# Optimization experiments

Hardware: AMD Instinct MI355X
Metric: run time of the kernel (lower is better)

## Reference

```python
import jax, jax.numpy as jnp
import numpy as np

V, D, NB, K, T = 32000, 256, 4, 8, 16


def setup_inputs() -> dict:
    key = jax.random.key(0)
    k0, k1, k2, k3, k4, k5 = jax.random.split(key, 6)
    tokens = jax.random.randint(k0, (T,), 0, V, dtype=jnp.int32)
    embed = jax.random.normal(k1, (V, D), jnp.float32) * 0.02
    W = jax.random.normal(k2, (K, D, D), jnp.float32) / np.float32(np.sqrt(D))
    bubbles = jax.random.normal(k3, (K, NB, D), jnp.float32) * 1.5  # init_spread_foam scale=1.5
    # scalars = [noise_gate_logit, self_temperature_logit, memory_decay_base, novelty_sensitivity]
    scalars = jax.random.normal(k4, (4,), jnp.float32)
    noise = jax.random.normal(k5, (T, K, NB, D), jnp.float32)  # per-step per-foam perturbations
    return {"tokens": tokens, "embed": embed, "W": W, "bubbles": bubbles,
            "scalars": scalars, "noise": noise}


def reference(tokens, embed, W, bubbles, scalars, noise):
    noise_gate = jax.nn.sigmoid(scalars[0])
    temp = jnp.maximum(jnp.abs(scalars[1]), 0.01)   # self_temperature
    decay_base = scalars[2]                          # memory_decay_base
    sensitivity = jnp.abs(scalars[3])                # novelty_sensitivity
    nb = bubbles.shape[1]

    def step(memory, inp):                           # memory: (K, NB, D)
        tok, pert = inp
        x = embed[tok]                               # (D,)
        mm = memory.mean(axis=1)                     # (K, D) memory mean per foam
        mem_norm = jnp.linalg.norm(mm, axis=-1) + 1e-10
        x_norm = jnp.linalg.norm(x) + 1e-10
        dot = mm @ x                                 # (K,)
        novelty = jnp.where(mem_norm > 1e-8, 1.0 - dot / (x_norm * mem_norm), 1.0)
        decay = jax.nn.sigmoid(decay_base - sensitivity * novelty)   # (K,)
        xwm = x[None, :] + decay[:, None] * mm                        # (K, D)
        state_scale = jnp.linalg.norm(xwm, axis=-1) + 1e-10           # (K,)
        # LevyFoam equilibrium (stand-in): small per-foam matmul + bubble offsets
        eq = jnp.tanh(jnp.einsum('kd,kde->ke', xwm, W))[:, None, :] + bubbles  # (K, NB, D)
        eq = eq + noise_gate * pert * state_scale[:, None, None] * 0.01
        new_mem = decay[:, None, None] * memory + (1.0 - decay)[:, None, None] * eq
        m = eq / (jnp.linalg.norm(eq, axis=-1, keepdims=True) + 1e-10)
        rho = jnp.einsum('kbd,kbe->kde', m, m) / nb                   # (K, D, D)
        purity = jnp.sum(rho * jnp.swapaxes(rho, 1, 2), axis=(1, 2))  # tr(rho @ rho)
        w = jax.nn.softmax(purity / temp)                             # (K,)
        rho_self = jnp.einsum('k,kde->de', w, rho)                    # (D, D)
        eig = jnp.clip(jnp.linalg.eigvalsh(rho_self), 1e-12, None)
        eig = eig / eig.sum()
        # born rule over full vocab: diag(E rho E^T)
        logits = jnp.sum((embed @ rho_self) * embed, axis=-1)         # (V,)
        logp = jax.nn.log_softmax(logits)
        probs = jnp.exp(logp)
        S_rho = -jnp.sum(eig * jnp.clip(jnp.log(eig), -100.0, None))
        H_tok = -jnp.sum(probs * jnp.clip(logp, -100.0, None))
        return new_mem, (probs, rho_self, S_rho, H_tok, purity, w)

    mem0 = jnp.zeros((W.shape[0], nb, embed.shape[1]), embed.dtype)
    _, outs = jax.lax.scan(step, mem0, (tokens, noise))
    token_probs, rhos, S_rho, H_tokens, purities, weights = outs
    return token_probs, rhos, S_rho, H_tokens, purities, weights
```

## Files before the change

### kernel.cpp

```cpp
#include <hip/hip_runtime.h>
#include <hip/hip_fp16.h>

#define VV 32000
#define DD 256
#define TT 16

#define OUT_PROBS 0
#define OUT_RHO   512000
#define OUT_SRHO  1560576
#define OUT_H     1560592
#define OUT_PUR   1560608
#define OUT_W     1560672

#define WS_MS    0
#define WS_MSBF  65536
#define WS_G     98304
#define WS_MAXP  102400
#define WS_SUMP  106496
#define WS_C     110592
#define WS_EBF   131072

#define LAMZ 5.3e-4f

typedef __attribute__((ext_vector_type(8))) short s8v;
typedef __attribute__((ext_vector_type(8))) _Float16 h8v;
typedef __attribute__((ext_vector_type(4))) float f4v;

__device__ __forceinline__ unsigned short f2bf(float f) {
  unsigned u = __float_as_uint(f);
  u += 0x7fffu + ((u >> 16) & 1u);
  return (unsigned short)(u >> 16);
}

__device__ __forceinline__ float fast_sigmoid(float z) {
  return __builtin_amdgcn_rcpf(1.f + __expf(-z));
}
__device__ __forceinline__ float fast_tanh(float y) {
  return 1.f - 2.f * __builtin_amdgcn_rcpf(__expf(2.f * y) + 1.f);
}

__global__ __launch_bounds__(512, 1) void k_chains(
    const int* __restrict__ tokens, const float* __restrict__ embed,
    const float* __restrict__ W, const float* __restrict__ bubbles,
    const float* __restrict__ scalars, const float* __restrict__ noise,
    float* __restrict__ out, float* __restrict__ ws,
    unsigned short* __restrict__ ebf) {
  const int k = blockIdx.x;
  const int tid = threadIdx.x;

  if (k >= 4) {
    const float4* src = (const float4*)embed;
    size_t start = (size_t)(k - 4) * 4000;
    if (ebf) {
      #pragma unroll 4
      for (int i = tid; i < 4000; i += 512) {
        float4 v = src[start + i];
        ushort4 o;
        o.x = f2bf(v.x); o.y = f2bf(v.y); o.z = f2bf(v.z); o.w = f2bf(v.w);
        *(ushort4*)(ebf + (size_t)(start + i) * 4) = o;
      }
    } else {
      float a = 0.f;
      #pragma unroll 4
      for (int i = tid; i < 4000; i += 512) {
        float4 v = src[start + i];
        a += v.x + v.y + v.z + v.w;
      }
      asm volatile("" :: "v"(a));
    }
    return;
  }

  __shared__ __align__(16) float erow[16 * 256];
  __shared__ __align__(16) float s_ms[64 * 256];
  __shared__ __align__(16) char  s_nz[32768];
  __shared__ __align__(16) float s_mmv[256];
  __shared__ __align__(16) float s_eq[256];
  __shared__ float s_rp[12];
  __shared__ float s_pp[40];
  __shared__ float s_pur[16];

  if (tid >= 256) {
    const int u = tid - 256;
    #pragma unroll 4
    for (int t = 0; t < TT; ++t) {
      const float* np = noise + (size_t)((t * 4 + k) * 4) * 256 + u;
      float n0 = np[0], n1 = np[256], n2 = np[512], n3 = np[768];
      uint64_t pk = (uint64_t)f2bf(n0) | ((uint64_t)f2bf(n1) << 16) |
                    ((uint64_t)f2bf(n2) << 32) | ((uint64_t)f2bf(n3) << 48);
      *(uint64_t*)(s_nz + ((t * 256 + u) << 3)) = pk;
    }
    #pragma unroll
    for (int it = 0; it < 4; ++it) {
      int f = it * 256 + u;
      int row = f >> 6, c4 = (f & 63) << 2;
      int tok = tokens[row];
      *(float4*)&erow[row * 256 + c4] = *(const float4*)(embed + (size_t)tok * DD + c4);
    }
    __syncthreads();
    return;
  }

  const int l = tid & 63, w = tid >> 6, lg = l >> 4;
  h8v Wreg[4][8];
  {
    const float* wp = W + (size_t)k * 65536 + (size_t)lg * 8 * 256 + w * 64 + (l & 15);
    #pragma unroll
    for (int nt = 0; nt < 4; ++nt) {
      #pragma unroll
      for (int kk = 0; kk < 8; ++kk) {
        h8v b;
        #pragma unroll
        for (int j = 0; j < 8; ++j)
          b[j] = (_Float16)wp[(kk * 32 + j) * 256 + nt * 16];
        Wreg[nt][kk] = b;
      }
    }
  }
  float bub0 = bubbles[(k * 4 + 0) * DD + tid];
  float bub1 = bubbles[(k * 4 + 1) * DD + tid];
  float bub2 = bubbles[(k * 4 + 2) * DD + tid];
  float bub3 = bubbles[(k * 4 + 3) * DD + tid];
  const float noise_gate = fast_sigmoid(scalars[0]);
  const float decay_base = scalars[2];
  const float sens = fabsf(scalars[3]);
  const float rowmask = ((l & 15) == 0) ? 1.f : 0.f;
  float mem0 = 0.f, mem1 = 0.f, mem2 = 0.f, mem3 = 0.f;
  __syncthreads();

  #pragma unroll 1
  for (int t = 0; t < TT; ++t) {
    float x = erow[t * 256 + tid];
    float mmv = 0.25f * (mem0 + mem1 + mem2 + mem3);
    s_mmv[tid] = mmv;
    float r0 = mmv * x, r1 = mmv * mmv, r2 = x * x;
    #pragma unroll
    for (int mm = 32; mm; mm >>= 1) {
      r0 += __shfl_xor(r0, mm);
      r1 += __shfl_xor(r1, mm);
      r2 += __shfl_xor(r2, mm);
    }
    if (l == 0) { s_rp[w * 3] = r0; s_rp[w * 3 + 1] = r1; s_rp[w * 3 + 2] = r2; }
    __syncthreads();
    float dot = s_rp[0] + s_rp[3] + s_rp[6] + s_rp[9];
    float mn  = s_rp[1] + s_rp[4] + s_rp[7] + s_rp[10];
    float xn  = s_rp[2] + s_rp[5] + s_rp[8] + s_rp[11];
    float mem_norm = sqrtf(mn) + 1e-10f;
    float x_norm = sqrtf(xn) + 1e-10f;
    float novelty = (mem_norm > 1e-8f) ? (1.f - dot / (x_norm * mem_norm)) : 1.f;
    float decay = fast_sigmoid(decay_base - sens * novelty);
    float ss2 = xn + 2.f * decay * dot + decay * decay * mn;
    float state_scale = sqrtf(ss2) + 1e-10f;
    float cns = noise_gate * state_scale * 0.01f;

    uint64_t pk = *(const uint64_t*)(s_nz + ((t * 256 + tid) << 3));
    float nz0 = __uint_as_float((uint32_t)(pk & 0xFFFFu) << 16);
    float nz1 = __uint_as_float((uint32_t)((pk >> 16) & 0xFFFFu) << 16);
    float nz2 = __uint_as_float((uint32_t)((pk >> 32) & 0xFFFFu) << 16);
    float nz3 = __uint_as_float((uint32_t)(pk >> 48) << 16);

    h8v afr[8];
    #pragma unroll
    for (int kk = 0; kk < 8; ++kk) {
      const float* mp_ = s_mmv + kk * 32 + lg * 8;
      const float* xp_ = erow + t * 256 + kk * 32 + lg * 8;
      float4 mv0 = *(const float4*)mp_, mv1 = *(const float4*)(mp_ + 4);
      float4 xv0 = *(const float4*)xp_, xv1 = *(const float4*)(xp_ + 4);
      h8v a;
      a[0] = (_Float16)(fmaf(decay, mv0.x, xv0.x) * rowmask);
      a[1] = (_Float16)(fmaf(decay, mv0.y, xv0.y) * rowmask);
      a[2] = (_Float16)(fmaf(decay, mv0.z, xv0.z) * rowmask);
      a[3] = (_Float16)(fmaf(decay, mv0.w, xv0.w) * rowmask);
      a[4] = (_Float16)(fmaf(decay, mv1.x, xv1.x) * rowmask);
      a[5] = (_Float16)(fmaf(decay, mv1.y, xv1.y) * rowmask);
      a[6] = (_Float16)(fmaf(decay, mv1.z, xv1.z) * rowmask);
      a[7] = (_Float16)(fmaf(decay, mv1.w, xv1.w) * rowmask);
      afr[kk] = a;
    }
    f4v acc[4];
    #pragma unroll
    for (int nt = 0; nt < 4; ++nt) acc[nt] = (f4v){0.f, 0.f, 0.f, 0.f};
    #pragma unroll
    for (int kk = 0; kk < 8; ++kk) {
      #pragma unroll
      for (int nt = 0; nt < 4; ++nt)
        acc[nt] = __builtin_amdgcn_mfma_f32_16x16x32_f16(afr[kk], Wreg[nt][kk], acc[nt], 0, 0, 0);
    }
    if (l < 16) {
      s_eq[w * 64 + 0 * 16 + l] = acc[0][0];
      s_eq[w * 64 + 1 * 16 + l] = acc[1][0];
      s_eq[w * 64 + 2 * 16 + l] = acc[2][0];
      s_eq[w * 64 + 3 * 16 + l] = acc[3][0];
    }
    asm volatile("s_waitcnt lgkmcnt(0)" ::: "memory");
    __builtin_amdgcn_sched_barrier(0);
    float th = fast_tanh(s_eq[tid]);
    float eq0 = th + bub0 + cns * nz0;
    float eq1 = th + bub1 + cns * nz1;
    float eq2 = th + bub2 + cns * nz2;
    float eq3 = th + bub3 + cns * nz3;
    float p[10];
    p[0] = eq0 * eq0; p[1] = eq0 * eq1; p[2] = eq0 * eq2; p[3] = eq0 * eq3;
    p[4] = eq1 * eq1; p[5] = eq1 * eq2; p[6] = eq1 * eq3;
    p[7] = eq2 * eq2; p[8] = eq2 * eq3; p[9] = eq3 * eq3;
    #pragma unroll
    for (int mm = 32; mm; mm >>= 1) {
      #pragma unroll
      for (int i = 0; i < 10; ++i) p[i] += __shfl_xor(p[i], mm);
    }
    if (l == 0) {
      #pragma unroll
      for (int i = 0; i < 10; ++i) s_pp[w * 10 + i] = p[i];
    }
    __syncthreads();
    float dots[10];
    #pragma unroll
    for (int i = 0; i < 10; ++i)
      dots[i] = s_pp[i] + s_pp[10 + i] + s_pp[20 + i] + s_pp[30 + i];
    float inv0 = __builtin_amdgcn_rcpf(sqrtf(dots[0]) + 1e-10f);
    float inv1 = __builtin_amdgcn_rcpf(sqrtf(dots[4]) + 1e-10f);
    float inv2 = __builtin_amdgcn_rcpf(sqrtf(dots[7]) + 1e-10f);
    float inv3 = __builtin_amdgcn_rcpf(sqrtf(dots[9]) + 1e-10f);
    s_ms[(t * 4 + 0) * 256 + tid] = eq0 * inv0;
    s_ms[(t * 4 + 1) * 256 + tid] = eq1 * inv1;
    s_ms[(t * 4 + 2) * 256 + tid] = eq2 * inv2;
    s_ms[(t * 4 + 3) * 256 + tid] = eq3 * inv3;
    float od = 1.f - decay;
    mem0 = decay * mem0 + od * eq0;
    mem1 = decay * mem1 + od * eq1;
    mem2 = decay * mem2 + od * eq2;
    mem3 = decay * mem3 + od * eq3;
    if (tid == 0) {
      float iv[4] = {inv0, inv1, inv2, inv3};
      float sum = 0.f; int c2 = 0;
      for (int b = 0; b < 4; ++b)
        for (int b2 = b; b2 < 4; ++b2) {
          float md = dots[c2] * iv[b] * iv[b2];
          float v = md * md;
          sum += (b2 == b) ? v : 2.f * v;
          ++c2;
        }
      s_pur[t] = sum * (1.f / 16.f);
    }
  }
  __syncthreads();
  #pragma unroll
  for (int it = 0; it < 16; ++it) {
    int r = it * 4 + w;
    int t = r >> 2, b = r & 3;
    float4 v = *(const float4*)&s_ms[r * 256 + l * 4];
    *(float4*)&ws[WS_MS + (((t * 16 + k * 4 + b) << 8)) + l * 4] = v;
  }
  if (tid < 16) out[OUT_PUR + tid * 4 + k] = s_pur[tid];
}

__global__ __launch_bounds__(256) void k_rho(const float* __restrict__ scalars,
                                             float* __restrict__ out,
                                             float* __restrict__ ws) {
  const int t = blockIdx.x >> 3, part = blockIdx.x & 7;
  const int e = threadIdx.x;
  __shared__ __align__(16) float Mlds[16 * 256];
  #pragma unroll
  for (int i = 0; i < 16; ++i) Mlds[i * DD + e] = ws[WS_MS + ((t * 16 + i) << 8) + e];
  float temp = fmaxf(fabsf(scalars[1]), 0.01f);
  float w[4]; float mx = -3.4e38f;
  for (int i = 0; i < 4; ++i) { w[i] = out[OUT_PUR + t * 4 + i] / temp; mx = fmaxf(mx, w[i]); }
  float sw = 0.f;
  for (int i = 0; i < 4; ++i) { w[i] = expf(w[i] - mx); sw += w[i]; }
  float iw = 1.f / sw;
  for (int i = 0; i < 4; ++i) w[i] *= iw;
  float c[16];
  #pragma unroll
  for (int i = 0; i < 16; ++i) c[i] = w[i >> 2] * 0.25f;
  __syncthreads();
  float mreg[16];
  #pragma unroll
  for (int i = 0; i < 16; ++i) mreg[i] = Mlds[i * DD + e];
  const int d0 = part * 32;
  for (int r = 0; r < 32; ++r) {
    int d = d0 + r;
    float a = 0.f;
    #pragma unroll
    for (int i = 0; i < 16; ++i) a = fmaf(c[i] * Mlds[i * DD + d], mreg[i], a);
    out[OUT_RHO + (size_t)t * 65536 + d * DD + e] = a;
  }
  if (part == 0) {
    unsigned short* msbf = (unsigned short*)(ws + WS_MSBF);
    #pragma unroll
    for (int i = 0; i < 16; ++i) msbf[(t * 16 + i) * DD + e] = f2bf(Mlds[i * DD + e]);
    if (e < 4) {
      out[OUT_W + t * 4 + e] = w[e];
      ws[WS_C + t * 4 + e] = w[e] * 0.25f;
    }
    if (e == 0) out[OUT_H + t] = 0.f;
    int gi = e >> 4, gj = e & 15;
    float g = 0.f;
    for (int d = 0; d < DD; ++d) {
      int dd = (d + gi * 16 + gj) & 255;
      g += Mlds[gi * DD + dd] * Mlds[gj * DD + dd];
    }
    ws[WS_G + t * 256 + e] = sqrtf(c[gi] * c[gj]) * g;
  }
}

template <int EBF>
__global__ __launch_bounds__(256) void k_big(const float* __restrict__ embed,
                                             const unsigned short* __restrict__ ebf,
                                             const float* __restrict__ scalars,
                                             float* __restrict__ out,
                                             float* __restrict__ ws) {
  const int bid = blockIdx.x;
  const int tid = threadIdx.x;
  __shared__ __align__(16) char smem[32768 + 2048];

  if (bid >= 16) {
    char* bbase = smem;
    float* Lt = (float*)(smem + 32768);
    int work = bid - 16;
    int wid = (work & 7) * 125 + (work >> 3);
    int vblk = wid >> 2, tg = wid & 3;
    int v0 = vblk * 128;

    const int lane = tid & 63, wv = tid >> 6;
    const int col = lane & 15, g = lane >> 4;

    s8v abf[2][8];
    if (EBF) {
      #pragma unroll
      for (int mt = 0; mt < 2; ++mt) {
        const s8v* ap = (const s8v*)(ebf + (size_t)(v0 + wv * 32 + mt * 16 + col) * 256);
        #pragma unroll
        for (int kk = 0; kk < 8; ++kk) abf[mt][kk] = ap[kk * 4 + g];
      }
    } else {
      #pragma unroll
      for (int mt = 0; mt < 2; ++mt) {
        const float* arow = embed + (size_t)(v0 + wv * 32 + mt * 16 + col) * DD + g * 8;
        #pragma unroll
        for (int kk = 0; kk < 8; ++kk) {
          float4 a0 = *(const float4*)(arow + kk * 32);
          float4 a1 = *(const float4*)(arow + kk * 32 + 4);
          s8v af;
          af[0] = (short)f2bf(a0.x); af[1] = (short)f2bf(a0.y);
          af[2] = (short)f2bf(a0.z); af[3] = (short)f2bf(a0.w);
          af[4] = (short)f2bf(a1.x); af[5] = (short)f2bf(a1.y);
          af[6] = (short)f2bf(a1.z); af[7] = (short)f2bf(a1.w);
          abf[mt][kk] = af;
        }
      }
    }
    const uint4* src = (const uint4*)((const char*)(ws + WS_MSBF) + tg * 32768);
    #pragma unroll
    for (int it = 0; it < 8; ++it) {
      int idx = it * 256 + tid;
      uint4 v = src[idx];
      int off = idx * 16;
      int phys = off ^ (((off >> 9) & 7) << 4);
      *(uint4*)(bbase + phys) = v;
    }
    float cfrag[4];
    #pragma unroll
    for (int nt = 0; nt < 4; ++nt)
      cfrag[nt] = ws[WS_C + (tg * 4 + nt) * 4 + (col >> 2)];
    __syncthreads();

    f4v acc[2][4];
    #pragma unroll
    for (int mt = 0; mt < 2; ++mt)
      #pragma unroll
      for (int nt = 0; nt < 4; ++nt) acc[mt][nt] = (f4v){0.f, 0.f, 0.f, 0.f};

    #pragma unroll
    for (int nt = 0; nt < 4; ++nt) {
      #pragma unroll
      for (int kk = 0; kk < 8; ++kk) {
        int brow = nt * 16 + col;
        int boff = brow * 512 + kk * 64 + g * 16;
        int bphys = boff ^ ((brow & 7) << 4);
        s8v bf = *reinterpret_cast<const s8v*>(bbase + bphys);
        acc[0][nt] = __builtin_amdgcn_mfma_f32_16x16x32_bf16(abf[0][kk], bf, acc[0][nt], 0, 0, 0);
        acc[1][nt] = __builtin_amdgcn_mfma_f32_16x16x32_bf16(abf[1][kk], bf, acc[1][nt], 0, 0, 0);
      }
    }

    #pragma unroll
    for (int mt = 0; mt < 2; ++mt) {
      #pragma unroll
      for (int nt = 0; nt < 4; ++nt) {
        float cv = cfrag[nt];
        float v4[4];
        #pragma unroll
        for (int j = 0; j < 4; ++j) {
          float v = acc[mt][nt][j];
          v = cv * v * v;
          v += __shfl_xor(v, 1); v += __shfl_xor(v, 2);
          v += __shfl_xor(v, 4); v += __shfl_xor(v, 8);
          v4[j] = v;
        }
        if (col == 0) {
          int rloc = wv * 32 + mt * 16 + g * 4;
          int t = tg * 4 + nt;
          float4 st = make_float4(v4[0], v4[1], v4[2], v4[3]);
          *(float4*)(&out[OUT_PROBS + (size_t)t * VV + v0 + rloc]) = st;
          *(float4*)(&Lt[nt * 128 + rloc]) = st;
        }
      }
    }
    __syncthreads();

    {
      float a = Lt[wv * 128 + lane], b = Lt[wv * 128 + 64 + lane];
      float m = fmaxf(a, b);
      #pragma unroll
      for (int msk = 32; msk; msk >>= 1) m = fmaxf(m, __shfl_xor(m, msk));
      float se = expf(a - m) + expf(b - m);
      #pragma unroll
      for (int msk = 32; msk; msk >>= 1) se += __shfl_xor(se, msk);
      if (lane == 0) {
        int t = tg * 4 + wv;
        ws[WS_MAXP + t * 256 + vblk] = m;
        ws[WS_SUMP + t * 256 + vblk] = se;
      }
    }
  } else {
    const int t = bid;
    float* Al = (float*)smem;
    int* ppt = (int*)(smem + 1024);
    Al[tid] = ws[WS_G + t * 256 + tid];
    if (tid < 120) {
      int r = tid >> 3, m = tid & 7;
      int a = (m == 0) ? 0 : 1 + (m - 1 + r) % 15;
      int b = 1 + (14 - m + r) % 15;
      ppt[r * 16 + a] = b;
      ppt[r * 16 + b] = a;
    }
    __syncthreads();
    const int i = tid >> 4, j = tid & 15;
    for (int sweep = 0; sweep < 5; ++sweep) {
      for (int r = 0; r < 15; ++r) {
        int pj = ppt[r * 16 + j], pi = ppt[r * 16 + i];
        float aj, bj, ai, bi;
        {
          int p = min(j, pj), q = max(j, pj);
          float apq = Al[p * 16 + q], app = Al[p * 17], aqq = Al[q * 17];
          float cc, sn;
          if (fabsf(apq) < 1e-30f) { cc = 1.f; sn = 0.f; }
          else {
            float tau = (aqq - app) / (2.f * apq);
            float tv = 1.f / (fabsf(tau) + sqrtf(1.f + tau * tau));
            if (tau < 0.f) tv = -tv;
            cc = 1.f / sqrtf(1.f + tv * tv);
            sn = tv * cc;
          }
          aj = cc; bj = (j == p) ? -sn : sn;
        }
        {
          int p = min(i, pi), q = max(i, pi);
          float apq = Al[p * 16 + q], app = Al[p * 17], aqq = Al[q * 17];
          float cc, sn;
          if (fabsf(apq) < 1e-30f) { cc = 1.f; sn = 0.f; }
          else {
            float tau = (aqq - app) / (2.f * apq);
            float tv = 1.f / (fabsf(tau) + sqrtf(1.f + tau * tau));
            if (tau < 0.f) tv = -tv;
            cc = 1.f / sqrtf(1.f + tv * tv);
            sn = tv * cc;
          }
          ai = cc; bi = (i == p) ? -sn : sn;
        }
        float nv = ai * aj * Al[i * 16 + j] + ai * bj * Al[i * 16 + pj] +
                   bi * aj * Al[pi * 16 + j] + bi * bj * Al[pi * 16 + pj];
        __syncthreads();
        Al[tid] = nv;
        __syncthreads();
      }
    }
    if (tid == 0) {
      float lam[16];
      float Z = 240.f * LAMZ;
      for (int q = 0; q < 16; ++q) { lam[q] = fmaxf(Al[q * 17], 1e-12f); Z += lam[q]; }
      float S = 0.f;
      for (int q = 0; q < 16; ++q) {
        float mu = lam[q] / Z;
        S -= mu * fmaxf(logf(mu), -100.f);
      }
      float muz = LAMZ / Z;
      S -= 240.f * muz * fmaxf(logf(muz), -100.f);
      out[OUT_SRHO + t] = S;
    }
  }
}

__global__ __launch_bounds__(256) void k_probs(float* __restrict__ out,
                                               float* __restrict__ ws) {
  const int bid = blockIdx.x;
  const int t = bid >> 5, chunk = bid & 31;
  const int tid = threadIdx.x;
  const int lane = tid & 63, wv = tid >> 6;
  __shared__ float red[4], red2[4], red3[4];

  float mp = (tid < 250) ? ws[WS_MAXP + t * 256 + tid] : -3.4e38f;
  float m = mp;
  #pragma unroll
  for (int msk = 32; msk; msk >>= 1) m = fmaxf(m, __shfl_xor(m, msk));
  if (lane == 0) red[wv] = m;
  __syncthreads();
  m = fmaxf(fmaxf(red[0], red[1]), fmaxf(red[2], red[3]));
  float se = (tid < 250) ? ws[WS_SUMP + t * 256 + tid] * expf(mp - m) : 0.f;
  #pragma unroll
  for (int msk = 32; msk; msk >>= 1) se += __shfl_xor(se, msk);
  if (lane == 0) red2[wv] = se;
  __syncthreads();
  const float lz = m + logf(red2[0] + red2[1] + red2[2] + red2[3]);

  float* pb = out + OUT_PROBS + (size_t)t * VV + chunk * 1000;
  float h = 0.f;
  for (int q = tid; q < 1000; q += 256) {
    float l = pb[q];
    float lp = l - lz;
    float p = expf(lp);
    pb[q] = p;
    h += p * fmaxf(lp, -100.f);
  }
  #pragma unroll
  for (int msk = 32; msk; msk >>= 1) h += __shfl_xor(h, msk);
  if (lane == 0) red3[wv] = h;
  __syncthreads();
  if (tid == 0) atomicAdd(&out[OUT_H + t], -(red3[0] + red3[1] + red3[2] + red3[3]));
}

extern "C" void kernel_launch(void* const* d_in, const int* in_sizes, int n_in,
                              void* d_out, int out_size, void* d_ws, size_t ws_size,
                              hipStream_t stream) {
  const int* tokens = (const int*)d_in[0];
  const float* embed = (const float*)d_in[1];
  const float* W = (const float*)d_in[2];
  const float* bub = (const float*)d_in[3];
  const float* sc = (const float*)d_in[4];
  const float* noise = (const float*)d_in[5];
  float* out = (float*)d_out;
  float* ws = (float*)d_ws;
  const size_t need = ((size_t)WS_EBF + 4096000) * 4;
  unsigned short* ebf = (ws_size >= need) ? (unsigned short*)(ws + WS_EBF) : nullptr;
  hipLaunchKernelGGL(k_chains, dim3(516), dim3(512), 0, stream,
                     tokens, embed, W, bub, sc, noise, out, ws, ebf);
  hipLaunchKernelGGL(k_rho, dim3(128), dim3(256), 0, stream, sc, out, ws);
  if (ebf)
    hipLaunchKernelGGL((k_big<1>), dim3(1016), dim3(256), 0, stream, embed, ebf, sc, out, ws);
  else
    hipLaunchKernelGGL((k_big<0>), dim3(1016), dim3(256), 0, stream, embed, ebf, sc, out, ws);
  hipLaunchKernelGGL(k_probs, dim3(512), dim3(256), 0, stream, out, ws);
}
```

Measured before the change: 133.1 us.

## Fuse rho kernel into logits kernel and double-buffer chain step reductions

Removes the separate k_rho launch. Its rho output, softmax weights and Gram-matrix work are folded into the big logits kernel as extra blocks, and the per-tile weight coefficients are recomputed from purity values instead of being read from workspace. The bf16 copy of the normalized bubbles is now written by k_chains. In the chain loop, the next step's memory-mean and norm reduction is computed before the existing barrier using double-buffered shared arrays, which saves one __syncthreads per step on the serial path. The cost is redundant softmax computation in many blocks and more work for the eigen blocks.

```diff
diff --git a/kernel.cpp b/kernel.cpp
--- a/kernel.cpp
+++ b/kernel.cpp
@@ -14,10 +14,8 @@
 
 #define WS_MS    0
 #define WS_MSBF  65536
-#define WS_G     98304
 #define WS_MAXP  102400
 #define WS_SUMP  106496
-#define WS_C     110592
 #define WS_EBF   131072
 
 #define LAMZ 5.3e-4f
@@ -74,10 +72,10 @@
   __shared__ __align__(16) float erow[16 * 256];
   __shared__ __align__(16) float s_ms[64 * 256];
   __shared__ __align__(16) char  s_nz[32768];
-  __shared__ __align__(16) float s_mmv[256];
+  __shared__ __align__(16) float s_mmv[2][256];
   __shared__ __align__(16) float s_eq[256];
-  __shared__ float s_rp[12];
-  __shared__ float s_pp[40];
+  __shared__ float s_rp[2][12];
+  __shared__ float s_pp[2][40];
   __shared__ float s_pur[16];
 
   if (tid >= 256) {
@@ -128,23 +126,22 @@
   float mem0 = 0.f, mem1 = 0.f, mem2 = 0.f, mem3 = 0.f;
   __syncthreads();
 
+  {
+    float x = erow[tid];
+    float r2 = x * x;
+    #pragma unroll
+    for (int mm = 32; mm; mm >>= 1) r2 += __shfl_xor(r2, mm);
+    if (l == 0) { s_rp[0][w * 3] = 0.f; s_rp[0][w * 3 + 1] = 0.f; s_rp[0][w * 3 + 2] = r2; }
+    s_mmv[0][tid] = 0.f;
+    __syncthreads();
+  }
+
   #pragma unroll 1
   for (int t = 0; t < TT; ++t) {
-    float x = erow[t * 256 + tid];
-    float mmv = 0.25f * (mem0 + mem1 + mem2 + mem3);
-    s_mmv[tid] = mmv;
-    float r0 = mmv * x, r1 = mmv * mmv, r2 = x * x;
-    #pragma unroll
-    for (int mm = 32; mm; mm >>= 1) {
-      r0 += __shfl_xor(r0, mm);
-      r1 += __shfl_xor(r1, mm);
-      r2 += __shfl_xor(r2, mm);
-    }
-    if (l == 0) { s_rp[w * 3] = r0; s_rp[w * 3 + 1] = r1; s_rp[w * 3 + 2] = r2; }
-    __syncthreads();
-    float dot = s_rp[0] + s_rp[3] + s_rp[6] + s_rp[9];
-    float mn  = s_rp[1] + s_rp[4] + s_rp[7] + s_rp[10];
-    float xn  = s_rp[2] + s_rp[5] + s_rp[8] + s_rp[11];
+    const int p = t & 1;
+    float dot = s_rp[p][0] + s_rp[p][3] + s_rp[p][6] + s_rp[p][9];
+    float mn  = s_rp[p][1] + s_rp[p][4] + s_rp[p][7] + s_rp[p][10];
+    float xn  = s_rp[p][2] + s_rp[p][5] + s_rp[p][8] + s_rp[p][11];
     float mem_norm = sqrtf(mn) + 1e-10f;
     float x_norm = sqrtf(xn) + 1e-10f;
     float novelty = (mem_norm > 1e-8f) ? (1.f - dot / (x_norm * mem_norm)) : 1.f;
@@ -162,7 +159,7 @@
     h8v afr[8];
     #pragma unroll
     for (int kk = 0; kk < 8; ++kk) {
-      const float* mp_ = s_mmv + kk * 32 + lg * 8;
+      const float* mp_ = &s_mmv[p][kk * 32 + lg * 8];
       const float* xp_ = erow + t * 256 + kk * 32 + lg * 8;
       float4 mv0 = *(const float4*)mp_, mv1 = *(const float4*)(mp_ + 4);
       float4 xv0 = *(const float4*)xp_, xv1 = *(const float4*)(xp_ + 4);
@@ -199,24 +196,44 @@
     float eq1 = th + bub1 + cns * nz1;
     float eq2 = th + bub2 + cns * nz2;
     float eq3 = th + bub3 + cns * nz3;
-    float p[10];
-    p[0] = eq0 * eq0; p[1] = eq0 * eq1; p[2] = eq0 * eq2; p[3] = eq0 * eq3;
-    p[4] = eq1 * eq1; p[5] = eq1 * eq2; p[6] = eq1 * eq3;
-    p[7] = eq2 * eq2; p[8] = eq2 * eq3; p[9] = eq3 * eq3;
+    float pr[10];
+    pr[0] = eq0 * eq0; pr[1] = eq0 * eq1; pr[2] = eq0 * eq2; pr[3] = eq0 * eq3;
+    pr[4] = eq1 * eq1; pr[5] = eq1 * eq2; pr[6] = eq1 * eq3;
+    pr[7] = eq2 * eq2; pr[8] = eq2 * eq3; pr[9] = eq3 * eq3;
     #pragma unroll
     for (int mm = 32; mm; mm >>= 1) {
       #pragma unroll
-      for (int i = 0; i < 10; ++i) p[i] += __shfl_xor(p[i], mm);
+      for (int i = 0; i < 10; ++i) pr[i] += __shfl_xor(pr[i], mm);
     }
     if (l == 0) {
       #pragma unroll
-      for (int i = 0; i < 10; ++i) s_pp[w * 10 + i] = p[i];
+      for (int i = 0; i < 10; ++i) s_pp[p][w * 10 + i] = pr[i];
+    }
+    float od = 1.f - decay;
+    mem0 = decay * mem0 + od * eq0;
+    mem1 = decay * mem1 + od * eq1;
+    mem2 = decay * mem2 + od * eq2;
+    mem3 = decay * mem3 + od * eq3;
+    if (t < 15) {
+      float xN = erow[(t + 1) * 256 + tid];
+      float mmvN = 0.25f * (mem0 + mem1 + mem2 + mem3);
+      s_mmv[p ^ 1][tid] = mmvN;
+      float q0 = mmvN * xN, q1 = mmvN * mmvN, q2 = xN * xN;
+      #pragma unroll
+      for (int mm = 32; mm; mm >>= 1) {
+        q0 += __shfl_xor(q0, mm);
+        q1 += __shfl_xor(q1, mm);
+        q2 += __shfl_xor(q2, mm);
+      }
+      if (l == 0) {
+        s_rp[p ^ 1][w * 3] = q0; s_rp[p ^ 1][w * 3 + 1] = q1; s_rp[p ^ 1][w * 3 + 2] = q2;
+      }
     }
     __syncthreads();
     float dots[10];
     #pragma unroll
     for (int i = 0; i < 10; ++i)
-      dots[i] = s_pp[i] + s_pp[10 + i] + s_pp[20 + i] + s_pp[30 + i];
+      dots[i] = s_pp[p][i] + s_pp[p][10 + i] + s_pp[p][20 + i] + s_pp[p][30 + i];
     float inv0 = __builtin_amdgcn_rcpf(sqrtf(dots[0]) + 1e-10f);
     float inv1 = __builtin_amdgcn_rcpf(sqrtf(dots[4]) + 1e-10f);
     float inv2 = __builtin_amdgcn_rcpf(sqrtf(dots[7]) + 1e-10f);
@@ -225,11 +242,6 @@
     s_ms[(t * 4 + 1) * 256 + tid] = eq1 * inv1;
     s_ms[(t * 4 + 2) * 256 + tid] = eq2 * inv2;
     s_ms[(t * 4 + 3) * 256 + tid] = eq3 * inv3;
-    float od = 1.f - decay;
-    mem0 = decay * mem0 + od * eq0;
-    mem1 = decay * mem1 + od * eq1;
-    mem2 = decay * mem2 + od * eq2;
-    mem3 = decay * mem3 + od * eq3;
     if (tid == 0) {
       float iv[4] = {inv0, inv1, inv2, inv3};
       float sum = 0.f; int c2 = 0;
@@ -244,76 +256,33 @@
     }
   }
   __syncthreads();
+  unsigned short* msbf = (unsigned short*)(ws + WS_MSBF);
   #pragma unroll
   for (int it = 0; it < 16; ++it) {
     int r = it * 4 + w;
     int t = r >> 2, b = r & 3;
     float4 v = *(const float4*)&s_ms[r * 256 + l * 4];
-    *(float4*)&ws[WS_MS + (((t * 16 + k * 4 + b) << 8)) + l * 4] = v;
+    int dst = ((t * 16 + k * 4 + b) << 8) + l * 4;
+    *(float4*)&ws[WS_MS + dst] = v;
+    ushort4 o;
+    o.x = f2bf(v.x); o.y = f2bf(v.y); o.z = f2bf(v.z); o.w = f2bf(v.w);
+    *(ushort4*)(msbf + dst) = o;
   }
   if (tid < 16) out[OUT_PUR + tid * 4 + k] = s_pur[tid];
 }
 
-__global__ __launch_bounds__(256) void k_rho(const float* __restrict__ scalars,
-                                             float* __restrict__ out,
-                                             float* __restrict__ ws) {
-  const int t = blockIdx.x >> 3, part = blockIdx.x & 7;
-  const int e = threadIdx.x;
-  __shared__ __align__(16) float Mlds[16 * 256];
-  #pragma unroll
-  for (int i = 0; i < 16; ++i) Mlds[i * DD + e] = ws[WS_MS + ((t * 16 + i) << 8) + e];
-  float temp = fmaxf(fabsf(scalars[1]), 0.01f);
-  float w[4]; float mx = -3.4e38f;
-  for (int i = 0; i < 4; ++i) { w[i] = out[OUT_PUR + t * 4 + i] / temp; mx = fmaxf(mx, w[i]); }
-  float sw = 0.f;
-  for (int i = 0; i < 4; ++i) { w[i] = expf(w[i] - mx); sw += w[i]; }
-  float iw = 1.f / sw;
-  for (int i = 0; i < 4; ++i) w[i] *= iw;
-  float c[16];
-  #pragma unroll
-  for (int i = 0; i < 16; ++i) c[i] = w[i >> 2] * 0.25f;
-  __syncthreads();
-  float mreg[16];
-  #pragma unroll
-  for (int i = 0; i < 16; ++i) mreg[i] = Mlds[i * DD + e];
-  const int d0 = part * 32;
-  for (int r = 0; r < 32; ++r) {
-    int d = d0 + r;
-    float a = 0.f;
-    #pragma unroll
-    for (int i = 0; i < 16; ++i) a = fmaf(c[i] * Mlds[i * DD + d], mreg[i], a);
-    out[OUT_RHO + (size_t)t * 65536 + d * DD + e] = a;
-  }
-  if (part == 0) {
-    unsigned short* msbf = (unsigned short*)(ws + WS_MSBF);
-    #pragma unroll
-    for (int i = 0; i < 16; ++i) msbf[(t * 16 + i) * DD + e] = f2bf(Mlds[i * DD + e]);
-    if (e < 4) {
-      out[OUT_W + t * 4 + e] = w[e];
-      ws[WS_C + t * 4 + e] = w[e] * 0.25f;
-    }
-    if (e == 0) out[OUT_H + t] = 0.f;
-    int gi = e >> 4, gj = e & 15;
-    float g = 0.f;
-    for (int d = 0; d < DD; ++d) {
-      int dd = (d + gi * 16 + gj) & 255;
-      g += Mlds[gi * DD + dd] * Mlds[gj * DD + dd];
-    }
-    ws[WS_G + t * 256 + e] = sqrtf(c[gi] * c[gj]) * g;
-  }
-}
-
 template <int EBF>
-__global__ __launch_bounds__(256) void k_big(const float* __restrict__ embed,
-                                             const unsigned short* __restrict__ ebf,
-                                             const float* __restrict__ scalars,
-                                             float* __restrict__ out,
-                                             float* __restrict__ ws) {
+__global__ __launch_bounds__(256) void k_mega(const float* __restrict__ embed,
+                                              const unsigned short* __restrict__ ebf,
+                                              const float* __restrict__ scalars,
+                                              float* __restrict__ out,
+                                              float* __restrict__ ws) {
   const int bid = blockIdx.x;
   const int tid = threadIdx.x;
   __shared__ __align__(16) char smem[32768 + 2048];
-
-  if (bid >= 16) {
+  const float temp = fmaxf(fabsf(scalars[1]), 0.01f);
+
+  if (bid >= 16 && bid < 1016) {
     char* bbase = smem;
     float* Lt = (float*)(smem + 32768);
     int work = bid - 16;
@@ -360,8 +329,14 @@
     }
     float cfrag[4];
     #pragma unroll
-    for (int nt = 0; nt < 4; ++nt)
-      cfrag[nt] = ws[WS_C + (tg * 4 + nt) * 4 + (col >> 2)];
+    for (int nt = 0; nt < 4; ++nt) {
+      int tq = tg * 4 + nt;
+      float pv[4]; float mx = -3.4e38f;
+      for (int i = 0; i < 4; ++i) { pv[i] = out[OUT_PUR + tq * 4 + i] / temp; mx = fmaxf(mx, pv[i]); }
+      float sw = 0.f;
+      for (int i = 0; i < 4; ++i) { pv[i] = expf(pv[i] - mx); sw += pv[i]; }
+      cfrag[nt] = pv[col >> 2] / sw * 0.25f;
+    }
     __syncthreads();
 
     f4v acc[2][4];
@@ -422,11 +397,19 @@
         ws[WS_SUMP + t * 256 + vblk] = se;
       }
     }
-  } else {
+  } else if (bid < 16) {
     const int t = bid;
     float* Al = (float*)smem;
     int* ppt = (int*)(smem + 1024);
-    Al[tid] = ws[WS_G + t * 256 + tid];
+    float* Ml = (float*)(smem + 2048);
+    #pragma unroll
+    for (int i = 0; i < 16; ++i) Ml[i * 256 + tid] = ws[WS_MS + ((t * 16 + i) << 8) + tid];
+    float w4[4]; float mx = -3.4e38f;
+    for (int i = 0; i < 4; ++i) { w4[i] = out[OUT_PUR + t * 4 + i] / temp; mx = fmaxf(mx, w4[i]); }
+    float sw = 0.f;
+    for (int i = 0; i < 4; ++i) { w4[i] = expf(w4[i] - mx); sw += w4[i]; }
+    float iw = 1.f / sw;
+    for (int i = 0; i < 4; ++i) w4[i] *= iw;
     if (tid < 120) {
       int r = tid >> 3, m = tid & 7;
       int a = (m == 0) ? 0 : 1 + (m - 1 + r) % 15;
@@ -435,7 +418,18 @@
       ppt[r * 16 + b] = a;
     }
     __syncthreads();
-    const int i = tid >> 4, j = tid & 15;
+    const int gi = tid >> 4, gj = tid & 15;
+    {
+      float g = 0.f;
+      for (int d = 0; d < DD; ++d) {
+        int dd = (d + gi * 16 + gj) & 255;
+        g += Ml[gi * 256 + dd] * Ml[gj * 256 + dd];
+      }
+      float ci = w4[gi >> 2] * 0.25f, cj = w4[gj >> 2] * 0.25f;
+      Al[tid] = sqrtf(ci * cj) * g;
+    }
+    __syncthreads();
+    const int i = gi, j = gj;
     for (int sweep = 0; sweep < 5; ++sweep) {
       for (int r = 0; r < 15; ++r) {
         int pj = ppt[r * 16 + j], pi = ppt[r * 16 + i];
@@ -488,6 +482,38 @@
       S -= 240.f * muz * fmaxf(logf(muz), -100.f);
       out[OUT_SRHO + t] = S;
     }
+  } else {
+    int rb = bid - 1016;
+    const int t = rb >> 3, part = rb & 7;
+    const int e = tid;
+    float* Mlds = (float*)smem;
+    #pragma unroll
+    for (int i = 0; i < 16; ++i) Mlds[i * 256 + e] = ws[WS_MS + ((t * 16 + i) << 8) + e];
+    float w4[4]; float mx = -3.4e38f;
+    for (int i = 0; i < 4; ++i) { w4[i] = out[OUT_PUR + t * 4 + i] / temp; mx = fmaxf(mx, w4[i]); }
+    float sw = 0.f;
+    for (int i = 0; i < 4; ++i) { w4[i] = expf(w4[i] - mx); sw += w4[i]; }
+    float iw = 1.f / sw;
+    for (int i = 0; i < 4; ++i) w4[i] *= iw;
+    float c[16];
+    #pragma unroll
+    for (int i = 0; i < 16; ++i) c[i] = w4[i >> 2] * 0.25f;
+    __syncthreads();
+    float mreg[16];
+    #pragma unroll
+    for (int i = 0; i < 16; ++i) mreg[i] = Mlds[i * 256 + e];
+    const int d0 = part * 32;
+    for (int r = 0; r < 32; ++r) {
+      int d = d0 + r;
+      float a = 0.f;
+      #pragma unroll
+      for (int i = 0; i < 16; ++i) a = fmaf(c[i] * Mlds[i * 256 + d], mreg[i], a);
+      out[OUT_RHO + (size_t)t * 65536 + d * DD + e] = a;
+    }
+    if (part == 0) {
+      if (e < 4) out[OUT_W + t * 4 + e] = w4[e];
+      if (e == 0) out[OUT_H + t] = 0.f;
+    }
   }
 }
 
@@ -544,10 +570,9 @@
   unsigned short* ebf = (ws_size >= need) ? (unsigned short*)(ws + WS_EBF) : nullptr;
   hipLaunchKernelGGL(k_chains, dim3(516), dim3(512), 0, stream,
                      tokens, embed, W, bub, sc, noise, out, ws, ebf);
-  hipLaunchKernelGGL(k_rho, dim3(128), dim3(256), 0, stream, sc, out, ws);
   if (ebf)
-    hipLaunchKernelGGL((k_big<1>), dim3(1016), dim3(256), 0, stream, embed, ebf, sc, out, ws);
+    hipLaunchKernelGGL((k_mega<1>), dim3(1144), dim3(256), 0, stream, embed, ebf, sc, out, ws);
   else
-    hipLaunchKernelGGL((k_big<0>), dim3(1016), dim3(256), 0, stream, embed, ebf, sc, out, ws);
+    hipLaunchKernelGGL((k_mega<0>), dim3(1144), dim3(256), 0, stream, embed, ebf, sc, out, ws);
   hipLaunchKernelGGL(k_probs, dim3(512), dim3(256), 0, stream, out, ws);
 }
```

After: 127.2 us. -4.5%, faster.
